# Performance work log

Hardware: AMD Instinct MI355X
Metric: run time of the kernel (lower is better)

## Reference

```python
import jax, jax.numpy as jnp
import numpy as np

D_MODEL = 1024
N_HEADS = 16
HEAD_DIM = D_MODEL // N_HEADS


def setup_inputs() -> dict:
    key = jax.random.key(0)
    ks = jax.random.split(key, 11)
    B, S = 8, 1024
    scale = 1.0 / np.sqrt(D_MODEL)
    inp = {
        "query": jax.random.normal(ks[0], (B, S, D_MODEL), jnp.float32),
        "key": jax.random.normal(ks[1], (B, S, D_MODEL), jnp.float32),
        "value": jax.random.normal(ks[2], (B, S, D_MODEL), jnp.float32),
        "Wq": jax.random.normal(ks[3], (D_MODEL, D_MODEL), jnp.float32) * scale,
        "bq": jnp.zeros((D_MODEL,), jnp.float32),
        "Wk": jax.random.normal(ks[4], (D_MODEL, D_MODEL), jnp.float32) * scale,
        "bk": jnp.zeros((D_MODEL,), jnp.float32),
        "Wv": jax.random.normal(ks[5], (D_MODEL, D_MODEL), jnp.float32) * scale,
        "bv": jnp.zeros((D_MODEL,), jnp.float32),
        "Wo": jax.random.normal(ks[6], (D_MODEL, D_MODEL), jnp.float32) * scale,
        "bo": jnp.zeros((D_MODEL,), jnp.float32),
    }
    return inp


def reference(query, key, value, Wq, bq, Wk, bk, Wv, bv, Wo, bo):
    B, S, _ = query.shape
    # projections (torch Linear: x @ W.T + b)
    Q = query @ Wq.T + bq
    K = key @ Wk.T + bk
    V = value @ Wv.T + bv
    # [B, H, S, Dh]
    Q = Q.reshape(B, S, N_HEADS, HEAD_DIM).transpose(0, 2, 1, 3)
    K = K.reshape(B, S, N_HEADS, HEAD_DIM).transpose(0, 2, 1, 3)
    V = V.reshape(B, S, N_HEADS, HEAD_DIM).transpose(0, 2, 1, 3)
    scores = jnp.einsum("bhqd,bhkd->bhqk", Q, K) / np.sqrt(HEAD_DIM).astype(np.float32)
    attention = jax.nn.softmax(scores, axis=-1)
    context = jnp.einsum("bhqk,bhkd->bhqd", attention, V)
    context = context.transpose(0, 2, 1, 3).reshape(B, S, D_MODEL)
    output = context @ Wo.T + bo
    return output, attention
```

## Files before the change

kernel.cpp:

```cpp
#include <hip/hip_runtime.h>
#include <cstddef>

typedef _Float16 f16;
typedef f16 f16x8 __attribute__((ext_vector_type(8)));
typedef short s16x8 __attribute__((ext_vector_type(8)));
typedef short s16x4 __attribute__((ext_vector_type(4)));
typedef float f32x4 __attribute__((ext_vector_type(4)));

#define S_LEN 1024
#define NH 16
#define HD 64
#define MROWS 8192
#define WPLANE 1048576

__device__ __forceinline__ f32x4 mfma_f16(f16x8 a, f16x8 b, f32x4 c) {
  return __builtin_amdgcn_mfma_f32_16x16x32_f16(a, b, c, 0, 0, 0);
}
__device__ __forceinline__ short f2h(float x) {
  f16 h = (f16)x;
  return __builtin_bit_cast(short, h);
}

typedef const __attribute__((address_space(1))) unsigned int* as1_u32p;
typedef __attribute__((address_space(3))) unsigned int* as3_u32p;
__device__ __forceinline__ void gl_lds16(const short* g, short* l) {
  __builtin_amdgcn_global_load_lds((as1_u32p)(const void*)g,
                                   (as3_u32p)(void*)l, 16, 0, 0);
}

__global__ __launch_bounds__(256) void convw4_k(
    const float* __restrict__ W0, const float* __restrict__ W1,
    const float* __restrict__ W2, const float* __restrict__ W3,
    short* __restrict__ out) {
  const int wsel = blockIdx.y;
  const float* W = wsel == 0 ? W0 : (wsel == 1 ? W1 : (wsel == 2 ? W2 : W3));
  const int i = (blockIdx.x * 256 + threadIdx.x) * 8;
  const int n = i >> 10, kg = i & 1023;
  const int dst = (((n >> 7) * 32 + (kg >> 5)) * 128 + (n & 127)) * 32 + (kg & 31);
  float xs[8];
  *(float4*)&xs[0] = *(const float4*)&W[i];
  *(float4*)&xs[4] = *(const float4*)&W[i + 4];
  s16x8 H;
#pragma unroll
  for (int j = 0; j < 8; ++j) H[j] = f2h(xs[j]);
  *(s16x8*)&out[(size_t)wsel * WPLANE + dst] = H;
}

__global__ __launch_bounds__(256, 2) void qkvproj_k(
    const float* __restrict__ Aq, const float* __restrict__ Ak,
    const float* __restrict__ Av, const short* __restrict__ Wpl,
    const float* __restrict__ bq, const float* __restrict__ bk,
    const float* __restrict__ bv, short* __restrict__ Oq,
    short* __restrict__ Ok, short* __restrict__ Ovt) {
  __shared__ __align__(16) short Ah[128][40];
  __shared__ __align__(16) short Bh[128][32];
  const int pid = blockIdx.y;
  const float* Af = pid == 0 ? Aq : (pid == 1 ? Ak : Av);
  const float* bias = pid == 0 ? bq : (pid == 1 ? bk : bv);
  const short* Whi = Wpl + (size_t)pid * WPLANE;

  const int t = threadIdx.x, lane = t & 63, wid = t >> 6;
  const int wr = wid >> 1, wc = wid & 1;
  const int fr = lane & 15, fg = lane >> 4;
  const int bid = blockIdx.x;
  const int wg = (bid & 7) * 64 + (bid >> 3);
  const int bm = (wg >> 3) * 128, bn = (wg & 7) * 128;
  const int srow = t >> 1, sk = (t & 1) * 16;

  f32x4 acc[4][4] = {};

  for (int ks = 0; ks < 32; ++ks) {
    const int k0 = ks * 32;
    {
      const size_t boff = ((size_t)(bn >> 7) * 32 + ks) * 4096;
      const int c0 = wid * 2;
      gl_lds16(&Whi[boff + (size_t)c0 * 512 + lane * 8],       &Bh[0][0] + c0 * 512);
      gl_lds16(&Whi[boff + (size_t)(c0 + 1) * 512 + lane * 8], &Bh[0][0] + (c0 + 1) * 512);
    }
    {
      const float* ap = &Af[(size_t)(bm + srow) * 1024 + k0 + sk];
      float xs[16];
      *(float4*)&xs[0]  = *(const float4*)(ap);
      *(float4*)&xs[4]  = *(const float4*)(ap + 4);
      *(float4*)&xs[8]  = *(const float4*)(ap + 8);
      *(float4*)&xs[12] = *(const float4*)(ap + 12);
      s16x8 H0, H1;
#pragma unroll
      for (int j = 0; j < 8; ++j) { H0[j] = f2h(xs[j]); H1[j] = f2h(xs[8 + j]); }
      *(s16x8*)&Ah[srow][sk] = H0; *(s16x8*)&Ah[srow][sk + 8] = H1;
    }
    __syncthreads();
    f16x8 ah[4], bh[4];
#pragma unroll
    for (int f = 0; f < 4; ++f) {
      ah[f] = *(const f16x8*)&Ah[wr * 64 + f * 16 + fr][fg * 8];
      bh[f] = *(const f16x8*)&Bh[wc * 64 + f * 16 + fr][fg * 8];
    }
#pragma unroll
    for (int i = 0; i < 4; ++i)
#pragma unroll
      for (int j = 0; j < 4; ++j)
        acc[i][j] = mfma_f16(ah[i], bh[j], acc[i][j]);
    __syncthreads();
  }

#pragma unroll
  for (int i = 0; i < 4; ++i) {
#pragma unroll
    for (int j = 0; j < 4; ++j) {
      const int m0 = bm + wr * 64 + i * 16 + fg * 4;
      const int n  = bn + wc * 64 + j * 16 + fr;
      const float bb = bias[n];
      const int batch = m0 >> 10, s0 = m0 & 1023;
      const int h = n >> 6, d = n & 63;
      if (pid < 2) {
        short* O = pid == 0 ? Oq : Ok;
        const size_t base = ((size_t)(batch * NH + h) * S_LEN + s0) * HD + d;
#pragma unroll
        for (int r = 0; r < 4; ++r)
          O[base + (size_t)r * HD] = f2h(acc[i][j][r] + bb);
      } else {
        s16x4 pk;
#pragma unroll
        for (int r = 0; r < 4; ++r) pk[r] = f2h(acc[i][j][r] + bb);
        *(s16x4*)&Ovt[((size_t)(batch * NH + h) * HD + d) * S_LEN + s0] = pk;
      }
    }
  }
}

__global__ __launch_bounds__(256, 2) void oproj_k(
    const short* __restrict__ Ahi, const short* __restrict__ Whi,
    const float* __restrict__ bias, float* __restrict__ Of) {
  __shared__ __align__(16) short Ah[128][32];
  __shared__ __align__(16) short Bh[128][32];
  const int t = threadIdx.x, lane = t & 63, wid = t >> 6;
  const int wr = wid >> 1, wc = wid & 1;
  const int fr = lane & 15, fg = lane >> 4;
  const int bid = blockIdx.x;
  const int wg = (bid & 7) * 64 + (bid >> 3);
  const int bm = (wg >> 3) * 128, bn = (wg & 7) * 128;

  f32x4 acc[4][4] = {};

  for (int ks = 0; ks < 32; ++ks) {
    {
      const size_t boff = ((size_t)(bn >> 7) * 32 + ks) * 4096;
      const size_t aoff = ((size_t)(bm >> 7) * 32 + ks) * 4096;
      const int c0 = wid * 2;
      gl_lds16(&Whi[boff + (size_t)c0 * 512 + lane * 8],       &Bh[0][0] + c0 * 512);
      gl_lds16(&Whi[boff + (size_t)(c0 + 1) * 512 + lane * 8], &Bh[0][0] + (c0 + 1) * 512);
      gl_lds16(&Ahi[aoff + (size_t)c0 * 512 + lane * 8],       &Ah[0][0] + c0 * 512);
      gl_lds16(&Ahi[aoff + (size_t)(c0 + 1) * 512 + lane * 8], &Ah[0][0] + (c0 + 1) * 512);
    }
    __syncthreads();
    f16x8 ah[4], bh[4];
#pragma unroll
    for (int f = 0; f < 4; ++f) {
      ah[f] = *(const f16x8*)&Ah[wr * 64 + f * 16 + fr][fg * 8];
      bh[f] = *(const f16x8*)&Bh[wc * 64 + f * 16 + fr][fg * 8];
    }
#pragma unroll
    for (int i = 0; i < 4; ++i)
#pragma unroll
      for (int j = 0; j < 4; ++j)
        acc[i][j] = mfma_f16(ah[i], bh[j], acc[i][j]);
    __syncthreads();
  }

#pragma unroll
  for (int i = 0; i < 4; ++i) {
#pragma unroll
    for (int j = 0; j < 4; ++j) {
      const int m0 = bm + wr * 64 + i * 16 + fg * 4;
      const int n  = bn + wc * 64 + j * 16 + fr;
      const float bb = bias[n];
#pragma unroll
      for (int r = 0; r < 4; ++r)
        Of[(size_t)(m0 + r) * 1024 + n] = acc[i][j][r] + bb;
    }
  }
}

template <bool FUSE_PV>
__global__ __launch_bounds__(256) void attn_k(
    const short* __restrict__ Qp, const short* __restrict__ Kp,
    const short* __restrict__ Vt, float* __restrict__ attn,
    short* __restrict__ Cp) {
  __shared__ __align__(16) short Kh[64][72];
  __shared__ __align__(16) short Vs[FUSE_PV ? 64 : 1][72];
  __shared__ __align__(16) short Pt[FUSE_PV ? 64 : 1][72];
  __shared__ float sums[2][64];
  __shared__ float sinv[64];

  const int wg = blockIdx.x;
  const int w  = (wg & 7) * 256 + (wg >> 3);
  const int bh = w >> 4;
  const int qb = (w & 15) * 64;
  const int batch = bh >> 4, h = bh & 15;

  const int t = threadIdx.x, lane = t & 63, wid = t >> 6;
  const int wq = wid >> 1, wk = wid & 1;
  const int fr = lane & 15, fg = lane >> 4;
  const int srow = t >> 2, sc = (t & 3) * 16;

  f16x8 qh[2][2];
#pragma unroll
  for (int fm = 0; fm < 2; ++fm)
#pragma unroll
    for (int kc = 0; kc < 2; ++kc) {
      const size_t qa =
          ((size_t)bh * S_LEN + qb + wq * 32 + fm * 16 + fr) * HD + kc * 32 + fg * 8;
      qh[fm][kc] = *(const f16x8*)&Qp[qa];
    }

  float rs[2] = {};
  for (int kt = 0; kt < 16; ++kt) {
    const size_t kb = ((size_t)bh * S_LEN + kt * 64 + srow) * HD + sc;
    const s16x8 h0 = *(const s16x8*)&Kp[kb];
    const s16x8 h1 = *(const s16x8*)&Kp[kb + 8];
    *(s16x8*)&Kh[srow][sc] = h0; *(s16x8*)&Kh[srow][sc + 8] = h1;
    __syncthreads();
    f16x8 kh[2][2];
#pragma unroll
    for (int fn = 0; fn < 2; ++fn)
#pragma unroll
      for (int kc = 0; kc < 2; ++kc)
        kh[fn][kc] = *(const f16x8*)&Kh[wk * 32 + fn * 16 + fr][kc * 32 + fg * 8];
    f32x4 s4[2][2] = {};
#pragma unroll
    for (int fn = 0; fn < 2; ++fn)
#pragma unroll
      for (int fm = 0; fm < 2; ++fm)
#pragma unroll
        for (int kc = 0; kc < 2; ++kc)
          s4[fn][fm] = mfma_f16(kh[fn][kc], qh[fm][kc], s4[fn][fm]);
#pragma unroll
    for (int fn = 0; fn < 2; ++fn)
#pragma unroll
      for (int fm = 0; fm < 2; ++fm)
#pragma unroll
        for (int r = 0; r < 4; ++r)
          rs[fm] += __expf(s4[fn][fm][r] * 0.125f);
    __syncthreads();
  }
#pragma unroll
  for (int fm = 0; fm < 2; ++fm) {
    float v = rs[fm];
    v += __shfl_xor(v, 16); v += __shfl_xor(v, 32);
    if (fg == 0) sums[wk][wq * 32 + fm * 16 + fr] = v;
  }
  __syncthreads();
  if (t < 64) sinv[t] = 1.0f / (sums[0][t] + sums[1][t]);
  __syncthreads();

  float pinv[2];
#pragma unroll
  for (int fm = 0; fm < 2; ++fm) pinv[fm] = sinv[wq * 32 + fm * 16 + fr];

  f32x4 apv[2][2] = {};
  for (int kt = 0; kt < 16; ++kt) {
    {
      const size_t kb = ((size_t)bh * S_LEN + kt * 64 + srow) * HD + sc;
      const s16x8 h0 = *(const s16x8*)&Kp[kb];
      const s16x8 h1 = *(const s16x8*)&Kp[kb + 8];
      *(s16x8*)&Kh[srow][sc] = h0; *(s16x8*)&Kh[srow][sc + 8] = h1;
      if constexpr (FUSE_PV) {
        const short* vrow = Vt + ((size_t)bh * HD + srow) * S_LEN + kt * 64 + sc;
        const s16x8 v0 = *(const s16x8*)(vrow);
        const s16x8 v1 = *(const s16x8*)(vrow + 8);
        *(s16x8*)&Vs[srow][sc] = v0; *(s16x8*)&Vs[srow][sc + 8] = v1;
      }
    }
    __syncthreads();
    f16x8 kh[2][2];
#pragma unroll
    for (int fn = 0; fn < 2; ++fn)
#pragma unroll
      for (int kc = 0; kc < 2; ++kc)
        kh[fn][kc] = *(const f16x8*)&Kh[wk * 32 + fn * 16 + fr][kc * 32 + fg * 8];
    f32x4 s4[2][2] = {};
#pragma unroll
    for (int fn = 0; fn < 2; ++fn)
#pragma unroll
      for (int fm = 0; fm < 2; ++fm)
#pragma unroll
        for (int kc = 0; kc < 2; ++kc)
          s4[fn][fm] = mfma_f16(kh[fn][kc], qh[fm][kc], s4[fn][fm]);
#pragma unroll
    for (int fm = 0; fm < 2; ++fm) {
      const int q = qb + wq * 32 + fm * 16 + fr;
#pragma unroll
      for (int fn = 0; fn < 2; ++fn) {
        const int kbase = wk * 32 + fn * 16 + fg * 4;
        float4 e4;
        e4.x = __expf(s4[fn][fm][0] * 0.125f) * pinv[fm];
        e4.y = __expf(s4[fn][fm][1] * 0.125f) * pinv[fm];
        e4.z = __expf(s4[fn][fm][2] * 0.125f) * pinv[fm];
        e4.w = __expf(s4[fn][fm][3] * 0.125f) * pinv[fm];
        *(float4*)&attn[((size_t)bh * S_LEN + q) * S_LEN + kt * 64 + kbase] = e4;
        if constexpr (FUSE_PV) {
          s16x4 pk;
          pk[0] = f2h(e4.x); pk[1] = f2h(e4.y);
          pk[2] = f2h(e4.z); pk[3] = f2h(e4.w);
          *(s16x4*)&Pt[wq * 32 + fm * 16 + fr][kbase] = pk;
        }
      }
    }
    __syncthreads();
    if constexpr (FUSE_PV) {
      f16x8 af[2][2], bv[2][2];
#pragma unroll
      for (int f = 0; f < 2; ++f)
#pragma unroll
        for (int kc = 0; kc < 2; ++kc) {
          af[f][kc] = *(const f16x8*)&Pt[wq * 32 + f * 16 + fr][kc * 32 + fg * 8];
          bv[f][kc] = *(const f16x8*)&Vs[wk * 32 + f * 16 + fr][kc * 32 + fg * 8];
        }
#pragma unroll
      for (int i = 0; i < 2; ++i)
#pragma unroll
        for (int j = 0; j < 2; ++j)
#pragma unroll
          for (int kc = 0; kc < 2; ++kc)
            apv[i][j] = mfma_f16(af[i][kc], bv[j][kc], apv[i][j]);
      __syncthreads();
    }
  }

  if constexpr (FUSE_PV) {
#pragma unroll
    for (int i = 0; i < 2; ++i)
#pragma unroll
      for (int j = 0; j < 2; ++j) {
        const int s0 = qb + wq * 32 + i * 16 + fg * 4;
        const int d = h * HD + wk * 32 + j * 16 + fr;
#pragma unroll
        for (int r = 0; r < 4; ++r) {
          const int m = batch * S_LEN + s0 + r;
          const size_t idx =
              (((size_t)(m >> 7) * 32 + (d >> 5)) * 128 + (m & 127)) * 32 + (d & 31);
          Cp[idx] = f2h(apv[i][j][r]);
        }
      }
  }
}

__global__ __launch_bounds__(256) void pv2_k(
    const float* __restrict__ attn, const short* __restrict__ Vt,
    short* __restrict__ Cp) {
  __shared__ __align__(16) short At[64][72], Vs[64][72];
  const int wg = blockIdx.x;
  const int w  = (wg & 7) * 256 + (wg >> 3);
  const int bh = w >> 4;
  const int qb = (w & 15) * 64;
  const int batch = bh >> 4, h = bh & 15;
  const int t = threadIdx.x, lane = t & 63, wid = t >> 6;
  const int wq = wid >> 1, wd = wid & 1;
  const int fr = lane & 15, fg = lane >> 4;
  const int srow = t >> 2, sc = (t & 3) * 16;
  const float* arow = attn + ((size_t)bh * S_LEN + qb + srow) * S_LEN + sc;
  const short* vrow = Vt + ((size_t)bh * HD + srow) * S_LEN + sc;

  f32x4 acc[2][2] = {};
  for (int kt = 0; kt < 16; ++kt) {
    float xs[16];
    *(float4*)&xs[0]  = *(const float4*)(arow + kt * 64);
    *(float4*)&xs[4]  = *(const float4*)(arow + kt * 64 + 4);
    *(float4*)&xs[8]  = *(const float4*)(arow + kt * 64 + 8);
    *(float4*)&xs[12] = *(const float4*)(arow + kt * 64 + 12);
    s16x8 c0, c1;
#pragma unroll
    for (int j = 0; j < 8; ++j) { c0[j] = f2h(xs[j]); c1[j] = f2h(xs[8 + j]); }
    const s16x8 v0 = *(const s16x8*)(vrow + kt * 64);
    const s16x8 v1 = *(const s16x8*)(vrow + kt * 64 + 8);
    *(s16x8*)&At[srow][sc] = c0; *(s16x8*)&At[srow][sc + 8] = c1;
    *(s16x8*)&Vs[srow][sc] = v0; *(s16x8*)&Vs[srow][sc + 8] = v1;
    __syncthreads();
    f16x8 af[2][2], bv[2][2];
#pragma unroll
    for (int f = 0; f < 2; ++f)
#pragma unroll
      for (int kc = 0; kc < 2; ++kc) {
        af[f][kc] = *(const f16x8*)&At[wq * 32 + f * 16 + fr][kc * 32 + fg * 8];
        bv[f][kc] = *(const f16x8*)&Vs[wd * 32 + f * 16 + fr][kc * 32 + fg * 8];
      }
#pragma unroll
    for (int i = 0; i < 2; ++i)
#pragma unroll
      for (int j = 0; j < 2; ++j)
#pragma unroll
        for (int kc = 0; kc < 2; ++kc)
          acc[i][j] = mfma_f16(af[i][kc], bv[j][kc], acc[i][j]);
    __syncthreads();
  }

#pragma unroll
  for (int i = 0; i < 2; ++i)
#pragma unroll
    for (int j = 0; j < 2; ++j) {
      const int s0 = qb + wq * 32 + i * 16 + fg * 4;
      const int d = h * HD + wd * 32 + j * 16 + fr;
#pragma unroll
      for (int r = 0; r < 4; ++r) {
        const int m = batch * S_LEN + s0 + r;
        const size_t idx =
            (((size_t)(m >> 7) * 32 + (d >> 5)) * 128 + (m & 127)) * 32 + (d & 31);
        Cp[idx] = f2h(acc[i][j][r]);
      }
    }
}

extern "C" void kernel_launch(void* const* d_in, const int* in_sizes, int n_in,
                              void* d_out, int out_size, void* d_ws, size_t ws_size,
                              hipStream_t stream) {
  const float* query = (const float*)d_in[0];
  const float* key   = (const float*)d_in[1];
  const float* value = (const float*)d_in[2];
  const float* Wq    = (const float*)d_in[3];
  const float* bq    = (const float*)d_in[4];
  const float* Wk    = (const float*)d_in[5];
  const float* bk    = (const float*)d_in[6];
  const float* Wv    = (const float*)d_in[7];
  const float* bv    = (const float*)d_in[8];
  const float* Wo    = (const float*)d_in[9];
  const float* bo    = (const float*)d_in[10];

  float* out  = (float*)d_out;
  float* attn = out + (size_t)MROWS * 1024;

  short* qp = (short*)d_ws;
  short* kp = qp + 8388608;
  short* vt = kp + 8388608;
  short* w4 = vt + 8388608;
  short* cx = w4 + 4 * WPLANE;

  const size_t need_fused = ((size_t)4 * 8388608 + 4 * WPLANE) * sizeof(short);
  const bool fuse = ws_size >= need_fused;

  const dim3 blk(256);

  convw4_k<<<dim3(512, 4), blk, 0, stream>>>(Wq, Wk, Wv, Wo, w4);
  qkvproj_k<<<dim3(512, 3), blk, 0, stream>>>(query, key, value, w4,
                                              bq, bk, bv, qp, kp, vt);

  short* ctxPlane;
  if (fuse) {
    attn_k<true><<<dim3(2048), blk, 0, stream>>>(qp, kp, vt, attn, cx);
    ctxPlane = cx;
  } else {
    attn_k<false><<<dim3(2048), blk, 0, stream>>>(qp, kp, vt, attn, nullptr);
    pv2_k<<<dim3(2048), blk, 0, stream>>>(attn, vt, qp);
    ctxPlane = qp;
  }

  oproj_k<<<dim3(512), blk, 0, stream>>>(ctxPlane, w4 + 3 * WPLANE, bo, out);
}
```

Baseline: 385.6 us.

## Give each attention wave a full 64-key row tile with 128 queries per block

The attention kernel now processes 128 query rows per block (1024 blocks instead of 2048), with each wave owning 32 queries across all 64 keys of a tile. This halves redundant K/V tile loads per query and lets the softmax row-sum finish in registers, removing the shared-memory sum exchange and its two barriers. It also adds s_setprio around the MFMA loops and uses nontemporal loads for projection inputs and nontemporal stores for the attention matrix. The trade-off is higher register pressure and fewer blocks in the grid.

New measurement: 472.4 us. +22.5%, slower.

```diff
diff --git a/kernel.cpp b/kernel.cpp
--- a/kernel.cpp
+++ b/kernel.cpp
@@ -79,14 +79,15 @@
     }
     {
       const float* ap = &Af[(size_t)(bm + srow) * 1024 + k0 + sk];
-      float xs[16];
-      *(float4*)&xs[0]  = *(const float4*)(ap);
-      *(float4*)&xs[4]  = *(const float4*)(ap + 4);
-      *(float4*)&xs[8]  = *(const float4*)(ap + 8);
-      *(float4*)&xs[12] = *(const float4*)(ap + 12);
+      f32x4 x0 = __builtin_nontemporal_load((const f32x4*)(ap));
+      f32x4 x1 = __builtin_nontemporal_load((const f32x4*)(ap + 4));
+      f32x4 x2 = __builtin_nontemporal_load((const f32x4*)(ap + 8));
+      f32x4 x3 = __builtin_nontemporal_load((const f32x4*)(ap + 12));
       s16x8 H0, H1;
 #pragma unroll
-      for (int j = 0; j < 8; ++j) { H0[j] = f2h(xs[j]); H1[j] = f2h(xs[8 + j]); }
+      for (int j = 0; j < 4; ++j) { H0[j] = f2h(x0[j]); H0[4 + j] = f2h(x1[j]); }
+#pragma unroll
+      for (int j = 0; j < 4; ++j) { H1[j] = f2h(x2[j]); H1[4 + j] = f2h(x3[j]); }
       *(s16x8*)&Ah[srow][sk] = H0; *(s16x8*)&Ah[srow][sk + 8] = H1;
     }
     __syncthreads();
@@ -189,18 +190,15 @@
     short* __restrict__ Cp) {
   __shared__ __align__(16) short Kh[64][72];
   __shared__ __align__(16) short Vs[FUSE_PV ? 64 : 1][72];
-  __shared__ __align__(16) short Pt[FUSE_PV ? 64 : 1][72];
-  __shared__ float sums[2][64];
-  __shared__ float sinv[64];
+  __shared__ __align__(16) short Pt[FUSE_PV ? 128 : 1][72];
 
   const int wg = blockIdx.x;
-  const int w  = (wg & 7) * 256 + (wg >> 3);
-  const int bh = w >> 4;
-  const int qb = (w & 15) * 64;
+  const int w  = (wg & 7) * 128 + (wg >> 3);
+  const int bh = w >> 3;
+  const int qb = (w & 7) * 128;
   const int batch = bh >> 4, h = bh & 15;
 
-  const int t = threadIdx.x, lane = t & 63, wid = t >> 6;
-  const int wq = wid >> 1, wk = wid & 1;
+  const int t = threadIdx.x, lane = t & 63, wv = t >> 6;
   const int fr = lane & 15, fg = lane >> 4;
   const int srow = t >> 2, sc = (t & 3) * 16;
 
@@ -210,7 +208,7 @@
 #pragma unroll
     for (int kc = 0; kc < 2; ++kc) {
       const size_t qa =
-          ((size_t)bh * S_LEN + qb + wq * 32 + fm * 16 + fr) * HD + kc * 32 + fg * 8;
+          ((size_t)bh * S_LEN + qb + wv * 32 + fm * 16 + fr) * HD + kc * 32 + fg * 8;
       qh[fm][kc] = *(const f16x8*)&Qp[qa];
     }
 
@@ -221,22 +219,24 @@
     const s16x8 h1 = *(const s16x8*)&Kp[kb + 8];
     *(s16x8*)&Kh[srow][sc] = h0; *(s16x8*)&Kh[srow][sc + 8] = h1;
     __syncthreads();
-    f16x8 kh[2][2];
-#pragma unroll
-    for (int fn = 0; fn < 2; ++fn)
+    f16x8 kh[4][2];
+#pragma unroll
+    for (int fn = 0; fn < 4; ++fn)
 #pragma unroll
       for (int kc = 0; kc < 2; ++kc)
-        kh[fn][kc] = *(const f16x8*)&Kh[wk * 32 + fn * 16 + fr][kc * 32 + fg * 8];
-    f32x4 s4[2][2] = {};
-#pragma unroll
-    for (int fn = 0; fn < 2; ++fn)
+        kh[fn][kc] = *(const f16x8*)&Kh[fn * 16 + fr][kc * 32 + fg * 8];
+    f32x4 s4[4][2] = {};
+    __builtin_amdgcn_s_setprio(1);
+#pragma unroll
+    for (int fn = 0; fn < 4; ++fn)
 #pragma unroll
       for (int fm = 0; fm < 2; ++fm)
 #pragma unroll
         for (int kc = 0; kc < 2; ++kc)
           s4[fn][fm] = mfma_f16(kh[fn][kc], qh[fm][kc], s4[fn][fm]);
-#pragma unroll
-    for (int fn = 0; fn < 2; ++fn)
+    __builtin_amdgcn_s_setprio(0);
+#pragma unroll
+    for (int fn = 0; fn < 4; ++fn)
 #pragma unroll
       for (int fm = 0; fm < 2; ++fm)
 #pragma unroll
@@ -244,21 +244,15 @@
           rs[fm] += __expf(s4[fn][fm][r] * 0.125f);
     __syncthreads();
   }
+  float pinv[2];
 #pragma unroll
   for (int fm = 0; fm < 2; ++fm) {
     float v = rs[fm];
     v += __shfl_xor(v, 16); v += __shfl_xor(v, 32);
-    if (fg == 0) sums[wk][wq * 32 + fm * 16 + fr] = v;
-  }
-  __syncthreads();
-  if (t < 64) sinv[t] = 1.0f / (sums[0][t] + sums[1][t]);
-  __syncthreads();
-
-  float pinv[2];
-#pragma unroll
-  for (int fm = 0; fm < 2; ++fm) pinv[fm] = sinv[wq * 32 + fm * 16 + fr];
-
-  f32x4 apv[2][2] = {};
+    pinv[fm] = 1.0f / v;
+  }
+
+  f32x4 apv[2][4] = {};
   for (int kt = 0; kt < 16; ++kt) {
     {
       const size_t kb = ((size_t)bh * S_LEN + kt * 64 + srow) * HD + sc;
@@ -273,57 +267,65 @@
       }
     }
     __syncthreads();
-    f16x8 kh[2][2];
-#pragma unroll
-    for (int fn = 0; fn < 2; ++fn)
+    f16x8 kh[4][2];
+#pragma unroll
+    for (int fn = 0; fn < 4; ++fn)
 #pragma unroll
       for (int kc = 0; kc < 2; ++kc)
-        kh[fn][kc] = *(const f16x8*)&Kh[wk * 32 + fn * 16 + fr][kc * 32 + fg * 8];
-    f32x4 s4[2][2] = {};
-#pragma unroll
-    for (int fn = 0; fn < 2; ++fn)
+        kh[fn][kc] = *(const f16x8*)&Kh[fn * 16 + fr][kc * 32 + fg * 8];
+    f32x4 s4[4][2] = {};
+    __builtin_amdgcn_s_setprio(1);
+#pragma unroll
+    for (int fn = 0; fn < 4; ++fn)
 #pragma unroll
       for (int fm = 0; fm < 2; ++fm)
 #pragma unroll
         for (int kc = 0; kc < 2; ++kc)
           s4[fn][fm] = mfma_f16(kh[fn][kc], qh[fm][kc], s4[fn][fm]);
+    __builtin_amdgcn_s_setprio(0);
 #pragma unroll
     for (int fm = 0; fm < 2; ++fm) {
-      const int q = qb + wq * 32 + fm * 16 + fr;
-#pragma unroll
-      for (int fn = 0; fn < 2; ++fn) {
-        const int kbase = wk * 32 + fn * 16 + fg * 4;
-        float4 e4;
-        e4.x = __expf(s4[fn][fm][0] * 0.125f) * pinv[fm];
-        e4.y = __expf(s4[fn][fm][1] * 0.125f) * pinv[fm];
-        e4.z = __expf(s4[fn][fm][2] * 0.125f) * pinv[fm];
-        e4.w = __expf(s4[fn][fm][3] * 0.125f) * pinv[fm];
-        *(float4*)&attn[((size_t)bh * S_LEN + q) * S_LEN + kt * 64 + kbase] = e4;
+      const int q = qb + wv * 32 + fm * 16 + fr;
+#pragma unroll
+      for (int fn = 0; fn < 4; ++fn) {
+        const int kbase = fn * 16 + fg * 4;
+        f32x4 e4;
+        e4[0] = __expf(s4[fn][fm][0] * 0.125f) * pinv[fm];
+        e4[1] = __expf(s4[fn][fm][1] * 0.125f) * pinv[fm];
+        e4[2] = __expf(s4[fn][fm][2] * 0.125f) * pinv[fm];
+        e4[3] = __expf(s4[fn][fm][3] * 0.125f) * pinv[fm];
+        __builtin_nontemporal_store(
+            e4, (f32x4*)&attn[((size_t)bh * S_LEN + q) * S_LEN + kt * 64 + kbase]);
         if constexpr (FUSE_PV) {
           s16x4 pk;
-          pk[0] = f2h(e4.x); pk[1] = f2h(e4.y);
-          pk[2] = f2h(e4.z); pk[3] = f2h(e4.w);
-          *(s16x4*)&Pt[wq * 32 + fm * 16 + fr][kbase] = pk;
+          pk[0] = f2h(e4[0]); pk[1] = f2h(e4[1]);
+          pk[2] = f2h(e4[2]); pk[3] = f2h(e4[3]);
+          *(s16x4*)&Pt[wv * 32 + fm * 16 + fr][kbase] = pk;
         }
       }
     }
     __syncthreads();
     if constexpr (FUSE_PV) {
-      f16x8 af[2][2], bv[2][2];
+      f16x8 af[2][2], bv[4][2];
 #pragma unroll
       for (int f = 0; f < 2; ++f)
 #pragma unroll
-        for (int kc = 0; kc < 2; ++kc) {
-          af[f][kc] = *(const f16x8*)&Pt[wq * 32 + f * 16 + fr][kc * 32 + fg * 8];
-          bv[f][kc] = *(const f16x8*)&Vs[wk * 32 + f * 16 + fr][kc * 32 + fg * 8];
-        }
+        for (int kc = 0; kc < 2; ++kc)
+          af[f][kc] = *(const f16x8*)&Pt[wv * 32 + f * 16 + fr][kc * 32 + fg * 8];
+#pragma unroll
+      for (int j = 0; j < 4; ++j)
+#pragma unroll
+        for (int kc = 0; kc < 2; ++kc)
+          bv[j][kc] = *(const f16x8*)&Vs[j * 16 + fr][kc * 32 + fg * 8];
+      __builtin_amdgcn_s_setprio(1);
 #pragma unroll
       for (int i = 0; i < 2; ++i)
 #pragma unroll
-        for (int j = 0; j < 2; ++j)
+        for (int j = 0; j < 4; ++j)
 #pragma unroll
           for (int kc = 0; kc < 2; ++kc)
             apv[i][j] = mfma_f16(af[i][kc], bv[j][kc], apv[i][j]);
+      __builtin_amdgcn_s_setprio(0);
       __syncthreads();
     }
   }
@@ -332,9 +334,9 @@
 #pragma unroll
     for (int i = 0; i < 2; ++i)
 #pragma unroll
-      for (int j = 0; j < 2; ++j) {
-        const int s0 = qb + wq * 32 + i * 16 + fg * 4;
-        const int d = h * HD + wk * 32 + j * 16 + fr;
+      for (int j = 0; j < 4; ++j) {
+        const int s0 = qb + wv * 32 + i * 16 + fg * 4;
+        const int d = h * HD + j * 16 + fr;
 #pragma unroll
         for (int r = 0; r < 4; ++r) {
           const int m = batch * S_LEN + s0 + r;
@@ -446,10 +448,10 @@
 
   short* ctxPlane;
   if (fuse) {
-    attn_k<true><<<dim3(2048), blk, 0, stream>>>(qp, kp, vt, attn, cx);
+    attn_k<true><<<dim3(1024), blk, 0, stream>>>(qp, kp, vt, attn, cx);
     ctxPlane = cx;
   } else {
-    attn_k<false><<<dim3(2048), blk, 0, stream>>>(qp, kp, vt, attn, nullptr);
+    attn_k<false><<<dim3(1024), blk, 0, stream>>>(qp, kp, vt, attn, nullptr);
     pv2_k<<<dim3(2048), blk, 0, stream>>>(attn, vt, qp);
     ctxPlane = qp;
   }
```
